# Performance work log

Hardware: AMD Instinct MI355X
Metric: run time of the kernel (lower is better)

Reference implementation:

```python
import jax, jax.numpy as jnp
import numpy as np

D_MODEL = 1024
N_HEADS = 16
HEAD_DIM = D_MODEL // N_HEADS
NEG = -10000.0  # module uses -10000, not -inf


def setup_inputs() -> dict:
    key = jax.random.key(0)
    ks = jax.random.split(key, 8)
    B, T = 4, 2048
    q = jax.random.normal(ks[0], (B, T, D_MODEL), dtype=jnp.float32)
    k = jax.random.normal(ks[1], (B, T, D_MODEL), dtype=jnp.float32)
    v = jax.random.normal(ks[2], (B, T, D_MODEL), dtype=jnp.float32)
    attn_mask = jnp.ones((B, T), dtype=jnp.float32)
    # xavier_uniform for square [d, d] weights: limit = sqrt(6/(d+d))
    lim = float(np.sqrt(6.0 / (D_MODEL + D_MODEL)))
    Wq = jax.random.uniform(ks[3], (D_MODEL, D_MODEL), jnp.float32, -lim, lim)
    Wk = jax.random.uniform(ks[4], (D_MODEL, D_MODEL), jnp.float32, -lim, lim)
    Wv = jax.random.uniform(ks[5], (D_MODEL, D_MODEL), jnp.float32, -lim, lim)
    Wo = jax.random.uniform(ks[6], (D_MODEL, D_MODEL), jnp.float32, -lim, lim)
    return {"q": q, "k": k, "v": v, "attn_mask": attn_mask,
            "Wq": Wq, "Wk": Wk, "Wv": Wv, "Wo": Wo, "mask_future": 1}


def _split_heads(x):
    B, T, _ = x.shape
    return x.reshape(B, T, N_HEADS, HEAD_DIM).transpose(0, 2, 1, 3)  # [B,H,T,D]


def reference(q, k, v, attn_mask, Wq, Wk, Wv, Wo, mask_future):
    # torch Linear: y = x @ W.T  (weights stored [out, in])
    qh = _split_heads(jnp.einsum('btd,ed->bte', q, Wq))
    kh = _split_heads(jnp.einsum('btd,ed->bte', k, Wk))
    vh = _split_heads(jnp.einsum('btd,ed->bte', v, Wv))
    L, S = qh.shape[-2], kh.shape[-2]
    # dual scale: each of q and k scaled by 1/d**0.25
    scale = 1.0 / jnp.sqrt(jnp.sqrt(jnp.float32(HEAD_DIM)))
    scores = jnp.einsum('bhld,bhsd->bhls', qh * scale, kh * scale)
    if mask_future:
        causal_bias = jnp.triu(jnp.full((L, S), NEG, dtype=scores.dtype), k=1)
        scores = scores + causal_bias
    # padding mask: attn_mask [B, S] -> broadcast [B,1,1,S]; 0 entries -> -10000
    pad = attn_mask[:, None, None, :]
    scores = jnp.where(pad == 0, jnp.asarray(NEG, scores.dtype), scores)
    probs = jax.nn.softmax(scores, axis=-1)  # dropout p=0.0 -> identity
    ctx = jnp.einsum('bhls,bhsd->bhld', probs, vh)
    B = ctx.shape[0]
    ctx = ctx.transpose(0, 2, 1, 3).reshape(B, L, D_MODEL)
    return jnp.einsum('btd,ed->bte', ctx, Wo)
```

## Files before the change

### kernel.cpp

```cpp
#include <hip/hip_runtime.h>

typedef unsigned short u16;
typedef __attribute__((ext_vector_type(8))) _Float16 f16x8;
typedef __attribute__((ext_vector_type(2))) __fp16 fp16v2;
typedef __attribute__((ext_vector_type(4))) float f32x4;
typedef __attribute__((ext_vector_type(16))) float f32x16;

#define T_SEQ 2048
#define NH 16
#define DH 64
#define DM 1024
#define NEG2 (-14426.95f)
#define QS2 (0.42466089f)

__device__ __forceinline__ unsigned pk2(float a, float b) {
  union { fp16v2 v; unsigned u; } c;
  c.v = __builtin_amdgcn_cvt_pkrtz(a, b);
  return c.u;
}
__device__ __forceinline__ u16 f2h(float a) {
  union { _Float16 h; u16 u; } c; c.h = (_Float16)a; return c.u;
}

__device__ __forceinline__ void async_load16(const void* g, void* l) {
  __builtin_amdgcn_global_load_lds(
      (const __attribute__((address_space(1))) unsigned int*)(g),
      (__attribute__((address_space(3))) unsigned int*)(l), 16, 0, 0);
}

__global__ __launch_bounds__(256) void convert_all(
    const float* __restrict__ q, const float* __restrict__ k, const float* __restrict__ v,
    const float* __restrict__ Wq, const float* __restrict__ Wk, const float* __restrict__ Wv,
    const float* __restrict__ Wo, u16* __restrict__ xb, u16* __restrict__ wb) {
  int blk = blockIdx.x;
  const float* src; u16* dst;
  if (blk < 12288) {
    int s = blk >> 12;
    src = (s == 0) ? q : (s == 1) ? k : v;
    dst = xb + (size_t)s * 8388608u;
    blk &= 4095;
  } else {
    int s = (blk - 12288) >> 9;
    src = (s == 0) ? Wq : (s == 1) ? Wk : (s == 2) ? Wv : Wo;
    dst = wb + (size_t)s * 1048576u;
    blk = (blk - 12288) & 511;
  }
  size_t base = (size_t)blk * 2048 + (size_t)threadIdx.x * 8;
  float4 a = *(const float4*)(src + base);
  float4 b2 = *(const float4*)(src + base + 4);
  uint4 st;
  st.x = pk2(a.x, a.y); st.y = pk2(a.z, a.w);
  st.z = pk2(b2.x, b2.y); st.w = pk2(b2.z, b2.w);
  *(uint4*)(dst + base) = st;
}

__global__ __launch_bounds__(512) void gemm_qkv(const u16* __restrict__ A,
                                                const u16* __restrict__ Wqb,
                                                const u16* __restrict__ Wkb,
                                                const u16* __restrict__ Wvb,
                                                u16* __restrict__ Qh, u16* __restrict__ Kh,
                                                u16* __restrict__ VTh) {
  __shared__ char lds[73728];
  const int tid = threadIdx.x;
  const int wid = tid >> 6, lane = tid & 63;
  const int l32 = lane & 31, lh = lane >> 5;
  const int m0 = blockIdx.x * 256;
  const int n0 = blockIdx.y * 128;
  const int which = n0 >> 10;
  const int n0l = n0 & 1023;
  const u16* As = A + (size_t)which * 8388608u;
  const u16* Bw = (which == 0) ? Wqb : (which == 1) ? Wkb : Wvb;
  f32x16 acc[2][2] = {};

  const u16* gsrc[3]; int ldso[3];
#pragma unroll
  for (int u = 0; u < 3; ++u) {
    int c = wid * 3 + u;
    ldso[u] = c * 1024;
    if (c < 16)
      gsrc[u] = As + (size_t)(m0 + (c >> 1) * 32 + l32) * 1024 + (c & 1) * 16 + lh * 8;
    else {
      int cw = c - 16;
      gsrc[u] = Bw + (size_t)(n0l + (cw >> 1) * 32 + l32) * 1024 + (cw & 1) * 16 + lh * 8;
    }
  }

  const int rOff = (which < 2) ? 16384 : 0;
  const int cOff = 16384 - rOff;
  const int rgo = (which < 2) ? ((wid & 1) * 2) : ((wid >> 1) * 2);
  const int cgo = (which < 2) ? ((wid >> 1) * 2) : ((wid & 1) * 2);

#pragma unroll
  for (int u = 0; u < 3; ++u) async_load16(gsrc[u] + 0 * 32, lds + 0 * 24576 + ldso[u]);
#pragma unroll
  for (int u = 0; u < 3; ++u) async_load16(gsrc[u] + 1 * 32, lds + 1 * 24576 + ldso[u]);

  int slotc = 0, slotn = 2;
  for (int kt = 0; kt < 32; ++kt) {
    if (kt < 31) asm volatile("s_waitcnt vmcnt(3)" ::: "memory");
    else         asm volatile("s_waitcnt vmcnt(0)" ::: "memory");
    __builtin_amdgcn_s_barrier();
    asm volatile("" ::: "memory");
    char* bufc = lds + slotc * 24576;
    if (kt < 30) {
      char* bufn = lds + slotn * 24576;
      int ko = (kt + 2) * 32;
#pragma unroll
      for (int u = 0; u < 3; ++u) async_load16(gsrc[u] + ko, bufn + ldso[u]);
    }
    const char* rb = bufc + rOff;
    const char* cb = bufc + cOff;
    f16x8 r0[2], c0[2], r1[2], c1[2];
#pragma unroll
    for (int i = 0; i < 2; ++i) {
      r0[i] = *(const f16x8*)(rb + ((rgo + i) * 2 + 0) * 1024 + lane * 16);
      c0[i] = *(const f16x8*)(cb + ((cgo + i) * 2 + 0) * 1024 + lane * 16);
    }
#pragma unroll
    for (int i = 0; i < 2; ++i) {
      r1[i] = *(const f16x8*)(rb + ((rgo + i) * 2 + 1) * 1024 + lane * 16);
      c1[i] = *(const f16x8*)(cb + ((cgo + i) * 2 + 1) * 1024 + lane * 16);
    }
    __builtin_amdgcn_s_setprio(1);
#pragma unroll
    for (int i = 0; i < 2; ++i)
#pragma unroll
      for (int j = 0; j < 2; ++j)
        acc[i][j] = __builtin_amdgcn_mfma_f32_32x32x16_f16(r0[i], c0[j], acc[i][j], 0, 0, 0);
#pragma unroll
    for (int i = 0; i < 2; ++i)
#pragma unroll
      for (int j = 0; j < 2; ++j)
        acc[i][j] = __builtin_amdgcn_mfma_f32_32x32x16_f16(r1[i], c1[j], acc[i][j], 0, 0, 0);
    __builtin_amdgcn_s_setprio(0);
    slotc = (slotc == 2) ? 0 : slotc + 1;
    slotn = (slotn == 2) ? 0 : slotn + 1;
  }

  const float s = (which < 2) ? QS2 : 1.0f;
  const int b = m0 >> 11, t0 = m0 & 2047, h0 = n0l >> 6;
  __syncthreads();
  if (which < 2) {
#pragma unroll
    for (int i = 0; i < 2; ++i)
#pragma unroll
      for (int j = 0; j < 2; ++j) {
        int colb = (wid >> 1) * 64 + j * 32 + l32;
        int rowb = (wid & 1) * 64 + i * 32 + 4 * lh;
#pragma unroll
        for (int g = 0; g < 4; ++g) {
          uint2 pv;
          pv.x = pk2(acc[i][j][4 * g + 0] * s, acc[i][j][4 * g + 1] * s);
          pv.y = pk2(acc[i][j][4 * g + 2] * s, acc[i][j][4 * g + 3] * s);
          *(uint2*)(lds + colb * 264 + (rowb + 8 * g) * 2) = pv;
        }
      }
    __syncthreads();
    u16* O = which ? Kh : Qh;
#pragma unroll
    for (int p = 0; p < 8; ++p) {
      int row = p * 32 + (tid >> 4);
      int seg = tid & 15;
      uint4 val = *(const uint4*)(lds + row * 264 + seg * 16);
      int hl = seg >> 3, dh0 = (seg & 7) * 8;
      *(uint4*)(O + (((size_t)(b * NH + h0 + hl) * T_SEQ + t0 + row) << 6) + dh0) = val;
    }
  } else {
#pragma unroll
    for (int i = 0; i < 2; ++i)
#pragma unroll
      for (int j = 0; j < 2; ++j) {
        int colb = (wid & 1) * 64 + j * 32 + l32;
        int rowb = (wid >> 1) * 64 + i * 32 + 4 * lh;
#pragma unroll
        for (int g = 0; g < 4; ++g) {
          uint2 pv;
          pv.x = pk2(acc[i][j][4 * g + 0], acc[i][j][4 * g + 1]);
          pv.y = pk2(acc[i][j][4 * g + 2], acc[i][j][4 * g + 3]);
          *(uint2*)(lds + colb * 520 + (rowb + 8 * g) * 2) = pv;
        }
      }
    __syncthreads();
#pragma unroll
    for (int p = 0; p < 8; ++p) {
      int row = p * 16 + (tid >> 5);
      int seg = tid & 31;
      uint4 val = *(const uint4*)(lds + row * 520 + seg * 16);
      int h = h0 + (row >> 6), dh = row & 63;
      *(uint4*)(VTh + (((size_t)(b * NH + h) * DH + dh) << 11) + t0 + seg * 8) = val;
    }
  }
}

__global__ __launch_bounds__(512) void gemm_out(const u16* __restrict__ A,
                                                const u16* __restrict__ Bw,
                                                float* __restrict__ O) {
  __shared__ char lds[73728];
  const int tid = threadIdx.x;
  const int wid = tid >> 6, lane = tid & 63;
  const int l32 = lane & 31, lh = lane >> 5;
  const int m0 = blockIdx.x * 256, n0 = blockIdx.y * 128;
  f32x16 acc[2][2] = {};

  const u16* gsrc[3]; int ldso[3];
#pragma unroll
  for (int u = 0; u < 3; ++u) {
    int c = wid * 3 + u;
    ldso[u] = c * 1024;
    if (c < 16)
      gsrc[u] = A + (size_t)(m0 + (c >> 1) * 32 + l32) * 1024 + (c & 1) * 16 + lh * 8;
    else {
      int cw = c - 16;
      gsrc[u] = Bw + (size_t)(n0 + (cw >> 1) * 32 + l32) * 1024 + (cw & 1) * 16 + lh * 8;
    }
  }
  const int rgo = (wid >> 1) * 2, cgo = (wid & 1) * 2;

#pragma unroll
  for (int u = 0; u < 3; ++u) async_load16(gsrc[u] + 0 * 32, lds + 0 * 24576 + ldso[u]);
#pragma unroll
  for (int u = 0; u < 3; ++u) async_load16(gsrc[u] + 1 * 32, lds + 1 * 24576 + ldso[u]);

  int slotc = 0, slotn = 2;
  for (int kt = 0; kt < 32; ++kt) {
    if (kt < 31) asm volatile("s_waitcnt vmcnt(3)" ::: "memory");
    else         asm volatile("s_waitcnt vmcnt(0)" ::: "memory");
    __builtin_amdgcn_s_barrier();
    asm volatile("" ::: "memory");
    char* bufc = lds + slotc * 24576;
    if (kt < 30) {
      char* bufn = lds + slotn * 24576;
      int ko = (kt + 2) * 32;
#pragma unroll
      for (int u = 0; u < 3; ++u) async_load16(gsrc[u] + ko, bufn + ldso[u]);
    }
    const char* rb = bufc;
    const char* cb = bufc + 16384;
    f16x8 r0[2], c0[2], r1[2], c1[2];
#pragma unroll
    for (int i = 0; i < 2; ++i) {
      r0[i] = *(const f16x8*)(rb + ((rgo + i) * 2 + 0) * 1024 + lane * 16);
      c0[i] = *(const f16x8*)(cb + ((cgo + i) * 2 + 0) * 1024 + lane * 16);
    }
#pragma unroll
    for (int i = 0; i < 2; ++i) {
      r1[i] = *(const f16x8*)(rb + ((rgo + i) * 2 + 1) * 1024 + lane * 16);
      c1[i] = *(const f16x8*)(cb + ((cgo + i) * 2 + 1) * 1024 + lane * 16);
    }
    __builtin_amdgcn_s_setprio(1);
#pragma unroll
    for (int i = 0; i < 2; ++i)
#pragma unroll
      for (int j = 0; j < 2; ++j)
        acc[i][j] = __builtin_amdgcn_mfma_f32_32x32x16_f16(r0[i], c0[j], acc[i][j], 0, 0, 0);
#pragma unroll
    for (int i = 0; i < 2; ++i)
#pragma unroll
      for (int j = 0; j < 2; ++j)
        acc[i][j] = __builtin_amdgcn_mfma_f32_32x32x16_f16(r1[i], c1[j], acc[i][j], 0, 0, 0);
    __builtin_amdgcn_s_setprio(0);
    slotc = (slotc == 2) ? 0 : slotc + 1;
    slotn = (slotn == 2) ? 0 : slotn + 1;
  }
#pragma unroll
  for (int i = 0; i < 2; ++i)
#pragma unroll
    for (int j = 0; j < 2; ++j) {
      int col = n0 + (wid & 1) * 64 + j * 32 + l32;
      int rowb = m0 + (wid >> 1) * 64 + i * 32 + 4 * lh;
#pragma unroll
      for (int g = 0; g < 4; ++g)
#pragma unroll
        for (int rr = 0; rr < 4; ++rr)
          O[(size_t)(rowb + 8 * g + rr) * 1024 + col] = acc[i][j][4 * g + rr];
    }
}

__global__ __launch_bounds__(512) void attn_kernel(const u16* __restrict__ Qh,
                                                   const u16* __restrict__ Kh,
                                                   const u16* __restrict__ VTh,
                                                   const float* __restrict__ attn_mask,
                                                   const int* __restrict__ mfp,
                                                   u16* __restrict__ ctx) {
  __shared__ char kls[2][8192];
  __shared__ char vls[8192];
  __shared__ char pls[8][1024];
  __shared__ int mzf;

  const int tid = threadIdx.x;
  const int wid = tid >> 6, lane = tid & 63;
  const int lm = lane & 15, lq = lane >> 4;
  const int bid = blockIdx.x;
  const int bh_i = bid & 63;
  const int qt = 15 - (bid >> 6);
  const int b = bh_i >> 4, h = bh_i & 15;
  const int mf = *mfp;
  const size_t bh = (size_t)(b * NH + h);
  const u16* Qbh = Qh + bh * T_SEQ * DH;
  const u16* Kbh = Kh + bh * T_SEQ * DH;
  const u16* VTbh = VTh + bh * DH * T_SEQ;
  const float* amb = attn_mask + (size_t)b * T_SEQ;

  f16x8 onev;
#pragma unroll
  for (int i = 0; i < 8; ++i) onev[i] = (_Float16)1.0f;

  if (tid == 0) mzf = 0;
  __syncthreads();
  {
    int az = 0;
    for (int i = tid; i < T_SEQ; i += 512) az |= (amb[i] == 0.0f);
    if (az) mzf = 1;
  }
  __syncthreads();
  const int maskzero = mzf;

  const int qw = qt * 128 + wid * 16;
  f16x8 qf[2];
  qf[0] = *(const f16x8*)(Qbh + (size_t)(qw + lm) * DH + lq * 8);
  qf[1] = *(const f16x8*)(Qbh + (size_t)(qw + lm) * DH + 32 + lq * 8);

  f32x4 acc[4] = {};
  f32x4 accs = {};
  float mprev = -1e30f;

  const int nch = mf ? (qt + 1) * 2 : 32;
  async_load16(Kbh + (size_t)((wid >> 1) * 16 + lm) * DH + (wid & 1) * 32 + lq * 8,
               kls[0] + wid * 1024);

  for (int c = 0; c < nch; ++c) {
    const int s0 = c * 64;
    asm volatile("s_waitcnt vmcnt(0)" ::: "memory");
    __builtin_amdgcn_s_barrier();
    asm volatile("" ::: "memory");
    async_load16(VTbh + (size_t)((wid >> 1) * 16 + lm) * T_SEQ + s0 + (wid & 1) * 32 + lq * 8,
                 vls + wid * 1024);
    if (c + 1 < nch) {
      async_load16(Kbh + (size_t)(s0 + 64 + (wid >> 1) * 16 + lm) * DH + (wid & 1) * 32 + lq * 8,
                   kls[(c + 1) & 1] + wid * 1024);
    }
    const char* kcur = kls[c & 1];

    f32x4 sc[4];
    for (int st = 0; st < 4; ++st) {
      f32x4 z = {0.f, 0.f, 0.f, 0.f};
      sc[st] = z;
      for (int kk = 0; kk < 2; ++kk) {
        f16x8 kf = *(const f16x8*)(kcur + ((st * 2 + kk) * 64 + lane) * 16);
        sc[st] = __builtin_amdgcn_mfma_f32_16x16x32_f16(kf, qf[kk], sc[st], 0, 0, 0);
      }
    }
    if (maskzero) {
      for (int st = 0; st < 4; ++st) {
        f32x4 mb = *(const f32x4*)(amb + s0 + st * 16 + lq * 4);
        for (int r = 0; r < 4; ++r)
          if (mb[r] == 0.0f) sc[st][r] += NEG2;
      }
    }
    if (mf && (s0 + 64 > qw)) {
      int qg = qw + lm;
      for (int st = 0; st < 4; ++st)
        for (int r = 0; r < 4; ++r)
          if (s0 + st * 16 + lq * 4 + r > qg) sc[st][r] = NEG2;
    }
    float u0 = fmaxf(fmaxf(sc[0][0], sc[0][1]), sc[0][2]);
    float u1 = fmaxf(fmaxf(sc[0][3], sc[1][0]), sc[1][1]);
    float u2 = fmaxf(fmaxf(sc[1][2], sc[1][3]), sc[2][0]);
    float u3 = fmaxf(fmaxf(sc[2][1], sc[2][2]), sc[2][3]);
    float u4 = fmaxf(fmaxf(sc[3][0], sc[3][1]), sc[3][2]);
    float mx = fmaxf(fmaxf(fmaxf(u0, u1), u2), fmaxf(fmaxf(u3, u4), sc[3][3]));
    mx = fmaxf(mx, __shfl_xor(mx, 16));
    mx = fmaxf(mx, __shfl_xor(mx, 32));
    if (__ballot(mx > mprev + 8.0f) != 0ull) {
      float mn2 = fmaxf(mprev, mx);
      float alpha = exp2f(mprev - mn2);
      for (int r = 0; r < 4; ++r) {
        float ar = __shfl(alpha, lq * 4 + r);
        for (int nt = 0; nt < 4; ++nt) acc[nt][r] *= ar;
        accs[r] *= ar;
      }
      mprev = mn2;
    }
    for (int st = 0; st < 4; ++st)
      for (int r = 0; r < 4; ++r)
        sc[st][r] = exp2f(sc[st][r] - mprev);

    {
      char* pw = pls[wid];
      for (int st = 0; st < 2; ++st) {
        int lqp = (st & 1) * 2 + (lq >> 1);
        uint2 pv;
        pv.x = pk2(sc[st][0], sc[st][1]);
        pv.y = pk2(sc[st][2], sc[st][3]);
        *(uint2*)(pw + (lqp * 16 + lm) * 16 + (lq & 1) * 8) = pv;
      }
    }
    if (c + 1 < nch) asm volatile("s_waitcnt vmcnt(1)" ::: "memory");
    else             asm volatile("s_waitcnt vmcnt(0)" ::: "memory");
    asm volatile("s_waitcnt lgkmcnt(0)" ::: "memory");
    {
      f16x8 pf = *(const f16x8*)(pls[wid] + lane * 16);
      for (int nt = 0; nt < 4; ++nt) {
        f16x8 vf = *(const f16x8*)(vls + ((nt * 2 + 0) * 64 + lane) * 16);
        acc[nt] = __builtin_amdgcn_mfma_f32_16x16x32_f16(pf, vf, acc[nt], 0, 0, 0);
      }
      accs = __builtin_amdgcn_mfma_f32_16x16x32_f16(pf, onev, accs, 0, 0, 0);
    }
    {
      char* pw = pls[wid];
      for (int st = 2; st < 4; ++st) {
        int lqp = (st & 1) * 2 + (lq >> 1);
        uint2 pv;
        pv.x = pk2(sc[st][0], sc[st][1]);
        pv.y = pk2(sc[st][2], sc[st][3]);
        *(uint2*)(pw + (lqp * 16 + lm) * 16 + (lq & 1) * 8) = pv;
      }
    }
    asm volatile("s_waitcnt lgkmcnt(0)" ::: "memory");
    {
      f16x8 pf = *(const f16x8*)(pls[wid] + lane * 16);
      for (int nt = 0; nt < 4; ++nt) {
        f16x8 vf = *(const f16x8*)(vls + ((nt * 2 + 1) * 64 + lane) * 16);
        acc[nt] = __builtin_amdgcn_mfma_f32_16x16x32_f16(pf, vf, acc[nt], 0, 0, 0);
      }
      accs = __builtin_amdgcn_mfma_f32_16x16x32_f16(pf, onev, accs, 0, 0, 0);
    }
  }
  for (int r = 0; r < 4; ++r) {
    float ir = 1.0f / accs[r];
    int t = qw + lq * 4 + r;
    for (int nt = 0; nt < 4; ++nt)
      ctx[((size_t)(b * T_SEQ + t) * DM) + h * DH + nt * 16 + lm] = f2h(acc[nt][r] * ir);
  }
}

extern "C" void kernel_launch(void* const* d_in, const int* in_sizes, int n_in,
                              void* d_out, int out_size, void* d_ws, size_t ws_size,
                              hipStream_t stream) {
  const float* q = (const float*)d_in[0];
  const float* k = (const float*)d_in[1];
  const float* v = (const float*)d_in[2];
  const float* attn_mask = (const float*)d_in[3];
  const float* Wq = (const float*)d_in[4];
  const float* Wk = (const float*)d_in[5];
  const float* Wv = (const float*)d_in[6];
  const float* Wo = (const float*)d_in[7];
  const int* mf = (const int*)d_in[8];

  u16* ws = (u16*)d_ws;
  u16* qb  = ws;
  u16* wqb = ws + 3u * 8388608u;
  u16* wkb = wqb + 1048576u;
  u16* wvb = wkb + 1048576u;
  u16* wob = wvb + 1048576u;
  u16* Qh  = wob + 1048576u;
  u16* Kh  = Qh + 8388608u;
  u16* VTh = Kh + 8388608u;
  u16* ctxb = ws;

  convert_all<<<14336, 256, 0, stream>>>(q, k, v, Wq, Wk, Wv, Wo, qb, wqb);

  dim3 gq(32, 24);
  gemm_qkv<<<gq, 512, 0, stream>>>(qb, wqb, wkb, wvb, Qh, Kh, VTh);

  attn_kernel<<<1024, 512, 0, stream>>>(Qh, Kh, VTh, attn_mask, mf, ctxb);

  dim3 gg(32, 8);
  gemm_out<<<gg, 512, 0, stream>>>(ctxb, wob, (float*)d_out);
}
```

Measured before the change: 328.0 us.

## Fuse fp32-to-fp16 activation conversion into QKV GEMM load pipeline

The separate pass that converted q/k/v activations to fp16 in a workspace is removed; only the weights are still pre-converted. The QKV GEMM now loads fp32 activations into registers, converts them, and writes fp16 to LDS one stage ahead, while weights keep using async global-to-LDS loads. This avoids a full read/write round trip of about 100MB of activations. In exchange, each QKV block reads fp32 activations repeatedly (once per N-tile column, 8 times per projection), and the pipeline uses more registers and has extra LDS-write synchronization.

```diff
diff --git a/kernel.cpp b/kernel.cpp
--- a/kernel.cpp
+++ b/kernel.cpp
@@ -28,23 +28,15 @@
       (__attribute__((address_space(3))) unsigned int*)(l), 16, 0, 0);
 }
 
-__global__ __launch_bounds__(256) void convert_all(
-    const float* __restrict__ q, const float* __restrict__ k, const float* __restrict__ v,
-    const float* __restrict__ Wq, const float* __restrict__ Wk, const float* __restrict__ Wv,
-    const float* __restrict__ Wo, u16* __restrict__ xb, u16* __restrict__ wb) {
+__global__ __launch_bounds__(256) void convert_w(
+    const float* __restrict__ Wq, const float* __restrict__ Wk,
+    const float* __restrict__ Wv, const float* __restrict__ Wo,
+    u16* __restrict__ wb) {
   int blk = blockIdx.x;
-  const float* src; u16* dst;
-  if (blk < 12288) {
-    int s = blk >> 12;
-    src = (s == 0) ? q : (s == 1) ? k : v;
-    dst = xb + (size_t)s * 8388608u;
-    blk &= 4095;
-  } else {
-    int s = (blk - 12288) >> 9;
-    src = (s == 0) ? Wq : (s == 1) ? Wk : (s == 2) ? Wv : Wo;
-    dst = wb + (size_t)s * 1048576u;
-    blk = (blk - 12288) & 511;
-  }
+  int s = blk >> 9;
+  const float* src = (s == 0) ? Wq : (s == 1) ? Wk : (s == 2) ? Wv : Wo;
+  u16* dst = wb + (size_t)s * 1048576u;
+  blk &= 511;
   size_t base = (size_t)blk * 2048 + (size_t)threadIdx.x * 8;
   float4 a = *(const float4*)(src + base);
   float4 b2 = *(const float4*)(src + base + 4);
@@ -54,7 +46,9 @@
   *(uint4*)(dst + base) = st;
 }
 
-__global__ __launch_bounds__(512) void gemm_qkv(const u16* __restrict__ A,
+__global__ __launch_bounds__(512) void gemm_qkv(const float* __restrict__ Xq,
+                                                const float* __restrict__ Xk,
+                                                const float* __restrict__ Xv,
                                                 const u16* __restrict__ Wqb,
                                                 const u16* __restrict__ Wkb,
                                                 const u16* __restrict__ Wvb,
@@ -68,74 +62,94 @@
   const int n0 = blockIdx.y * 128;
   const int which = n0 >> 10;
   const int n0l = n0 & 1023;
-  const u16* As = A + (size_t)which * 8388608u;
+  const float* Xs = (which == 0) ? Xq : (which == 1) ? Xk : Xv;
   const u16* Bw = (which == 0) ? Wqb : (which == 1) ? Wkb : Wvb;
   f32x16 acc[2][2] = {};
 
-  const u16* gsrc[3]; int ldso[3];
-#pragma unroll
-  for (int u = 0; u < 3; ++u) {
-    int c = wid * 3 + u;
-    ldso[u] = c * 1024;
-    if (c < 16)
-      gsrc[u] = As + (size_t)(m0 + (c >> 1) * 32 + l32) * 1024 + (c & 1) * 16 + lh * 8;
-    else {
-      int cw = c - 16;
-      gsrc[u] = Bw + (size_t)(n0l + (cw >> 1) * 32 + l32) * 1024 + (cw & 1) * 16 + lh * 8;
-    }
-  }
+  const float* gx0 = Xs + (size_t)(m0 + wid * 32 + l32) * 1024 + lh * 8;
+  const float* gx1 = gx0 + 16;
+  const int ldsoX0 = (2 * wid) * 1024;
+  const int ldsoX1 = ldsoX0 + 1024;
+  const u16* gw = Bw + (size_t)(n0l + (wid >> 1) * 32 + l32) * 1024 + (wid & 1) * 16 + lh * 8;
+  const int ldsoW = 16384 + wid * 1024;
 
   const int rOff = (which < 2) ? 16384 : 0;
   const int cOff = 16384 - rOff;
   const int rgo = (which < 2) ? ((wid & 1) * 2) : ((wid >> 1) * 2);
   const int cgo = (which < 2) ? ((wid >> 1) * 2) : ((wid & 1) * 2);
 
-#pragma unroll
-  for (int u = 0; u < 3; ++u) async_load16(gsrc[u] + 0 * 32, lds + 0 * 24576 + ldso[u]);
-#pragma unroll
-  for (int u = 0; u < 3; ++u) async_load16(gsrc[u] + 1 * 32, lds + 1 * 24576 + ldso[u]);
-
-  int slotc = 0, slotn = 2;
-  for (int kt = 0; kt < 32; ++kt) {
-    if (kt < 31) asm volatile("s_waitcnt vmcnt(3)" ::: "memory");
-    else         asm volatile("s_waitcnt vmcnt(0)" ::: "memory");
-    __builtin_amdgcn_s_barrier();
-    asm volatile("" ::: "memory");
-    char* bufc = lds + slotc * 24576;
-    if (kt < 30) {
-      char* bufn = lds + slotn * 24576;
-      int ko = (kt + 2) * 32;
-#pragma unroll
-      for (int u = 0; u < 3; ++u) async_load16(gsrc[u] + ko, bufn + ldso[u]);
-    }
-    const char* rb = bufc + rOff;
-    const char* cb = bufc + cOff;
-    f16x8 r0[2], c0[2], r1[2], c1[2];
-#pragma unroll
-    for (int i = 0; i < 2; ++i) {
-      r0[i] = *(const f16x8*)(rb + ((rgo + i) * 2 + 0) * 1024 + lane * 16);
-      c0[i] = *(const f16x8*)(cb + ((cgo + i) * 2 + 0) * 1024 + lane * 16);
-    }
-#pragma unroll
-    for (int i = 0; i < 2; ++i) {
-      r1[i] = *(const f16x8*)(rb + ((rgo + i) * 2 + 1) * 1024 + lane * 16);
-      c1[i] = *(const f16x8*)(cb + ((cgo + i) * 2 + 1) * 1024 + lane * 16);
-    }
-    __builtin_amdgcn_s_setprio(1);
-#pragma unroll
-    for (int i = 0; i < 2; ++i)
-#pragma unroll
-      for (int j = 0; j < 2; ++j)
-        acc[i][j] = __builtin_amdgcn_mfma_f32_32x32x16_f16(r0[i], c0[j], acc[i][j], 0, 0, 0);
-#pragma unroll
-    for (int i = 0; i < 2; ++i)
-#pragma unroll
-      for (int j = 0; j < 2; ++j)
-        acc[i][j] = __builtin_amdgcn_mfma_f32_32x32x16_f16(r1[i], c1[j], acc[i][j], 0, 0, 0);
-    __builtin_amdgcn_s_setprio(0);
-    slotc = (slotc == 2) ? 0 : slotc + 1;
-    slotn = (slotn == 2) ? 0 : slotn + 1;
-  }
+  float4 xa0, xa1, xa2, xa3;
+  float4 xb0, xb1, xb2, xb3;
+  xa0 = *(const float4*)(gx0);      xa1 = *(const float4*)(gx0 + 4);
+  xa2 = *(const float4*)(gx1);      xa3 = *(const float4*)(gx1 + 4);
+  async_load16(gw, lds + 0 * 24576 + ldsoW);
+  xb0 = *(const float4*)(gx0 + 32); xb1 = *(const float4*)(gx0 + 36);
+  xb2 = *(const float4*)(gx1 + 32); xb3 = *(const float4*)(gx1 + 36);
+  async_load16(gw + 32, lds + 1 * 24576 + ldsoW);
+  {
+    uint4 p0, p1;
+    p0.x = pk2(xa0.x, xa0.y); p0.y = pk2(xa0.z, xa0.w);
+    p0.z = pk2(xa1.x, xa1.y); p0.w = pk2(xa1.z, xa1.w);
+    p1.x = pk2(xa2.x, xa2.y); p1.y = pk2(xa2.z, xa2.w);
+    p1.z = pk2(xa3.x, xa3.y); p1.w = pk2(xa3.z, xa3.w);
+    *(uint4*)(lds + ldsoX0 + lane * 16) = p0;
+    *(uint4*)(lds + ldsoX1 + lane * 16) = p1;
+  }
+  asm volatile("s_waitcnt lgkmcnt(0)" ::: "memory");
+
+#define QKV_BODY(KT, RL0, RL1, RL2, RL3, RW0, RW1, RW2, RW3)                     \
+  {                                                                              \
+    const int kt = (KT);                                                         \
+    if (kt < 31) asm volatile("s_waitcnt vmcnt(5)" ::: "memory");                \
+    else         asm volatile("s_waitcnt vmcnt(0)" ::: "memory");                \
+    __builtin_amdgcn_s_barrier();                                                \
+    asm volatile("" ::: "memory");                                               \
+    char* bufc = lds + (kt % 3) * 24576;                                         \
+    if (kt < 30) {                                                               \
+      char* bufn = lds + ((kt + 2) % 3) * 24576;                                 \
+      RL0 = *(const float4*)(gx0 + (kt + 2) * 32);                               \
+      RL1 = *(const float4*)(gx0 + (kt + 2) * 32 + 4);                           \
+      RL2 = *(const float4*)(gx1 + (kt + 2) * 32);                               \
+      RL3 = *(const float4*)(gx1 + (kt + 2) * 32 + 4);                           \
+      async_load16(gw + (kt + 2) * 32, bufn + ldsoW);                            \
+    }                                                                            \
+    const char* rb = bufc + rOff;                                                \
+    const char* cb = bufc + cOff;                                                \
+    f16x8 r0[2], c0[2], r1[2], c1[2];                                            \
+    for (int i = 0; i < 2; ++i) {                                                \
+      r0[i] = *(const f16x8*)(rb + ((rgo + i) * 2 + 0) * 1024 + lane * 16);      \
+      c0[i] = *(const f16x8*)(cb + ((cgo + i) * 2 + 0) * 1024 + lane * 16);      \
+    }                                                                            \
+    for (int i = 0; i < 2; ++i) {                                                \
+      r1[i] = *(const f16x8*)(rb + ((rgo + i) * 2 + 1) * 1024 + lane * 16);      \
+      c1[i] = *(const f16x8*)(cb + ((cgo + i) * 2 + 1) * 1024 + lane * 16);      \
+    }                                                                            \
+    __builtin_amdgcn_s_setprio(1);                                               \
+    for (int i = 0; i < 2; ++i)                                                  \
+      for (int j = 0; j < 2; ++j)                                                \
+        acc[i][j] = __builtin_amdgcn_mfma_f32_32x32x16_f16(r0[i], c0[j], acc[i][j], 0, 0, 0); \
+    for (int i = 0; i < 2; ++i)                                                  \
+      for (int j = 0; j < 2; ++j)                                                \
+        acc[i][j] = __builtin_amdgcn_mfma_f32_32x32x16_f16(r1[i], c1[j], acc[i][j], 0, 0, 0); \
+    __builtin_amdgcn_s_setprio(0);                                               \
+    if (kt < 31) {                                                               \
+      char* bufw = lds + ((kt + 1) % 3) * 24576;                                 \
+      uint4 p0, p1;                                                              \
+      p0.x = pk2(RW0.x, RW0.y); p0.y = pk2(RW0.z, RW0.w);                        \
+      p0.z = pk2(RW1.x, RW1.y); p0.w = pk2(RW1.z, RW1.w);                        \
+      p1.x = pk2(RW2.x, RW2.y); p1.y = pk2(RW2.z, RW2.w);                        \
+      p1.z = pk2(RW3.x, RW3.y); p1.w = pk2(RW3.z, RW3.w);                        \
+      *(uint4*)(bufw + ldsoX0 + lane * 16) = p0;                                 \
+      *(uint4*)(bufw + ldsoX1 + lane * 16) = p1;                                 \
+    }                                                                            \
+    asm volatile("s_waitcnt lgkmcnt(0)" ::: "memory");                           \
+  }
+
+  for (int kt2 = 0; kt2 < 32; kt2 += 2) {
+    QKV_BODY(kt2,     xa0, xa1, xa2, xa3, xb0, xb1, xb2, xb3);
+    QKV_BODY(kt2 + 1, xb0, xb1, xb2, xb3, xa0, xa1, xa2, xa3);
+  }
+#undef QKV_BODY
 
   const float s = (which < 2) ? QS2 : 1.0f;
   const int b = m0 >> 11, t0 = m0 & 2047, h0 = n0l >> 6;
@@ -448,7 +462,6 @@
   const int* mf = (const int*)d_in[8];
 
   u16* ws = (u16*)d_ws;
-  u16* qb  = ws;
   u16* wqb = ws + 3u * 8388608u;
   u16* wkb = wqb + 1048576u;
   u16* wvb = wkb + 1048576u;
@@ -458,10 +471,10 @@
   u16* VTh = Kh + 8388608u;
   u16* ctxb = ws;
 
-  convert_all<<<14336, 256, 0, stream>>>(q, k, v, Wq, Wk, Wv, Wo, qb, wqb);
+  convert_w<<<2048, 256, 0, stream>>>(Wq, Wk, Wv, Wo, wqb);
 
   dim3 gq(32, 24);
-  gemm_qkv<<<gq, 512, 0, stream>>>(qb, wqb, wkb, wvb, Qh, Kh, VTh);
+  gemm_qkv<<<gq, 512, 0, stream>>>(q, k, v, wqb, wkb, wvb, Qh, Kh, VTh);
 
   attn_kernel<<<1024, 512, 0, stream>>>(Qh, Kh, VTh, attn_mask, mf, ctxb);
 
```

Result: slower. 409.6 us (+24.9%).
